# Kernel tuning notes

Hardware: AMD Instinct MI355X
Metric: run time of the kernel (lower is better)

Reference implementation:

```python
import jax, jax.numpy as jnp
import numpy as np

B, C, H, W = 4, 256, 256, 256
P = 256            # num_points
THRESH = 0.8
EPS = 1e-5


def setup_inputs() -> dict:
    key = jax.random.key(0)
    ks = jax.random.split(key, 4)
    x = jax.random.normal(ks[0], (B, C, H, W), dtype=jnp.float32)
    edge = jax.random.uniform(ks[1], (B, 1, H, W), dtype=jnp.float32)
    # GCN params (Conv1d kernel_size=1, no bias) + eval-mode BatchNorm params
    w_adj = jax.random.normal(ks[2], (P, P), dtype=jnp.float32) * (1.0 / np.sqrt(P))
    w_wg = jax.random.normal(ks[3], (C, C), dtype=jnp.float32) * (1.0 / np.sqrt(C))
    return {
        "x": x, "edge": edge,
        "w_adj": w_adj,
        "g_adj": jnp.ones((P,), jnp.float32), "b_adj": jnp.zeros((P,), jnp.float32),
        "m_adj": jnp.zeros((P,), jnp.float32), "v_adj": jnp.ones((P,), jnp.float32),
        "w_wg": w_wg,
        "g_wg": jnp.ones((C,), jnp.float32), "b_wg": jnp.zeros((C,), jnp.float32),
        "m_wg": jnp.zeros((C,), jnp.float32), "v_wg": jnp.ones((C,), jnp.float32),
    }


def _bn(z, mean, var, gamma, beta):
    # eval-mode BatchNorm1d over axis 1 of (B, ch, L)
    inv = gamma / jnp.sqrt(var + EPS)
    return z * inv[None, :, None] + (beta - mean * inv)[None, :, None]


def reference(x, edge, w_adj, g_adj, b_adj, m_adj, v_adj,
              w_wg, g_wg, b_wg, m_wg, v_wg):
    Bx, Cx, Hx, Wx = x.shape
    HW = Hx * Wx
    # threshold boundary map, pick P most-uncertain grid points per image
    e = jnp.where(edge < THRESH, 0.0, edge).reshape(Bx, HW)
    _, idx = jax.lax.top_k(e, P)                      # (B, P) int32 indices into HW
    xf = x.reshape(Bx, Cx, HW)
    idx3 = jnp.broadcast_to(idx[:, None, :], (Bx, Cx, P))
    feat = jnp.take_along_axis(xf, idx3, axis=2)      # gather: (B, C, P)
    feat = feat.transpose(0, 2, 1)                    # (B, P, C) = (b, n, d)
    # GCN stage 1: adjacency mix over nodes + BN + ReLU + residual
    z = jnp.einsum('ij,bjd->bid', w_adj, feat)        # (B, P, C)
    z = jax.nn.relu(_bn(z, m_adj, v_adj, g_adj, b_adj)) + feat
    # GCN stage 2: feature transform + BN + ReLU
    zt = z.transpose(0, 2, 1)                         # (B, C, P)
    z2 = jnp.einsum('cd,bdp->bcp', w_wg, zt)          # (B, C, P)
    z2 = jax.nn.relu(_bn(z2, m_wg, v_wg, g_wg, b_wg))
    # scatter reasoned point features back into the grid (indices are unique per row)
    bi = jnp.arange(Bx)[:, None, None]
    ci = jnp.arange(Cx)[None, :, None]
    out = xf.at[bi, ci, idx3].set(z2)
    return out.reshape(Bx, Cx, Hx, Wx)
```

## Files before the change

### kernel.cpp

```cpp
#include <hip/hip_runtime.h>
#include <stdint.h>

#define HW_   65536
#define B_    4
#define C_    256
#define P_    256
#define TH_   0.8f
#define EPS_  1e-5f

#define CHUNK_  4096
#define NCHUNK_ (HW_ / CHUNK_)
#define NCAND_  (NCHUNK_ * P_)

__device__ __forceinline__ uint64_t make_key(float v, int i) {
    if (v < TH_) v = 0.0f;
    return ((uint64_t)__float_as_uint(v) << 32) | (uint32_t)(65535 - i);
}

__global__ __launch_bounds__(512) void topk_local_kernel(const float* __restrict__ edge,
                                                         uint64_t* __restrict__ cand) {
    __shared__ uint64_t sk[CHUNK_];
    const int b = blockIdx.y;
    const int chunk = blockIdx.x;
    const int tid = threadIdx.x;
    const int base = chunk * CHUNK_;
    for (int t = tid; t < CHUNK_; t += 512) {
        const int i = base + t;
        sk[t] = make_key(edge[b * HW_ + i], i);
    }
    __syncthreads();
    for (int k = 2; k <= CHUNK_; k <<= 1) {
        for (int j = k >> 1; j > 0; j >>= 1) {
            for (int t = tid; t < CHUNK_ / 2; t += 512) {
                const int i = 2 * t - (t & (j - 1));
                const int ixj = i + j;
                const uint64_t a = sk[i], c = sk[ixj];
                const bool desc = ((i & k) == 0);
                if (desc ? (a < c) : (a > c)) { sk[i] = c; sk[ixj] = a; }
            }
            __syncthreads();
        }
    }
    if (tid < 256) cand[(b * NCHUNK_ + chunk) * P_ + tid] = sk[tid];
}

__global__ __launch_bounds__(1024) void topk_merge_kernel(const uint64_t* __restrict__ cand,
                                                          int* __restrict__ idx_out) {
    __shared__ uint64_t sk[NCAND_];
    const int b = blockIdx.x;
    const int tid = threadIdx.x;
    for (int t = tid; t < NCAND_; t += 1024) sk[t] = cand[b * NCAND_ + t];
    __syncthreads();
    for (int k = 2; k <= NCAND_; k <<= 1) {
        for (int j = k >> 1; j > 0; j >>= 1) {
            for (int t = tid; t < NCAND_ / 2; t += 1024) {
                const int i = 2 * t - (t & (j - 1));
                const int ixj = i + j;
                const uint64_t a = sk[i], c = sk[ixj];
                const bool desc = ((i & k) == 0);
                if (desc ? (a < c) : (a > c)) { sk[i] = c; sk[ixj] = a; }
            }
            __syncthreads();
        }
    }
    if (tid < 256) idx_out[b * P_ + tid] = 65535 - (int)(sk[tid] & 0xFFFFFFFFull);
}

__global__ __launch_bounds__(256) void copy_kernel(const float4* __restrict__ src,
                                                   float4* __restrict__ dst, int n4) {
    int i = blockIdx.x * 256 + threadIdx.x;
    const int stride = gridDim.x * 256;
    for (; i < n4; i += stride) dst[i] = src[i];
}

__global__ __launch_bounds__(256) void gather_kernel(const float* __restrict__ x,
                                                     const int* __restrict__ idx,
                                                     float* __restrict__ feat) {
    const int bn = blockIdx.x;
    const int d = threadIdx.x;
    const int b = bn >> 8;
    const int hw = idx[bn];
    feat[(size_t)bn * C_ + d] = x[((size_t)(b * C_ + d)) * HW_ + hw];
}

__global__ __launch_bounds__(256) void mm1_kernel(const float* __restrict__ w_adj,
                                                  const float* __restrict__ feat,
                                                  const float* __restrict__ g,
                                                  const float* __restrict__ bb,
                                                  const float* __restrict__ m,
                                                  const float* __restrict__ vv,
                                                  float* __restrict__ z) {
    __shared__ __align__(16) float a_s[64][68];
    __shared__ __align__(16) float b_s[64][68];
    const int b = blockIdx.y;
    const int i0 = (blockIdx.x >> 2) * 64;
    const int d0 = (blockIdx.x & 3) * 64;
    const int tid = threadIdx.x;
    const int tx = tid & 15, ty = tid >> 4;
    const float* fb = feat + (size_t)b * P_ * C_;

    float acc[4][4] = {};
    for (int k0 = 0; k0 < 256; k0 += 64) {
        for (int l = tid; l < 4096; l += 256) {
            int r = l >> 6, c = l & 63;
            a_s[r][c] = w_adj[(i0 + r) * 256 + (k0 + c)];
            b_s[r][c] = fb[(size_t)(k0 + r) * 256 + (d0 + c)];
        }
        __syncthreads();
        #pragma unroll
        for (int kk = 0; kk < 64; kk += 4) {
            float4 a4[4], b4[4];
            #pragma unroll
            for (int r = 0; r < 4; ++r) a4[r] = *(const float4*)&a_s[ty * 4 + r][kk];
            #pragma unroll
            for (int j = 0; j < 4; ++j) b4[j] = *(const float4*)&b_s[kk + j][tx * 4];
            #pragma unroll
            for (int r = 0; r < 4; ++r) {
                const float4 av = a4[r];
                const float aj0 = av.x, aj1 = av.y, aj2 = av.z, aj3 = av.w;
                acc[r][0] = fmaf(aj0, b4[0].x, acc[r][0]);
                acc[r][1] = fmaf(aj0, b4[0].y, acc[r][1]);
                acc[r][2] = fmaf(aj0, b4[0].z, acc[r][2]);
                acc[r][3] = fmaf(aj0, b4[0].w, acc[r][3]);
                acc[r][0] = fmaf(aj1, b4[1].x, acc[r][0]);
                acc[r][1] = fmaf(aj1, b4[1].y, acc[r][1]);
                acc[r][2] = fmaf(aj1, b4[1].z, acc[r][2]);
                acc[r][3] = fmaf(aj1, b4[1].w, acc[r][3]);
                acc[r][0] = fmaf(aj2, b4[2].x, acc[r][0]);
                acc[r][1] = fmaf(aj2, b4[2].y, acc[r][1]);
                acc[r][2] = fmaf(aj2, b4[2].z, acc[r][2]);
                acc[r][3] = fmaf(aj2, b4[2].w, acc[r][3]);
                acc[r][0] = fmaf(aj3, b4[3].x, acc[r][0]);
                acc[r][1] = fmaf(aj3, b4[3].y, acc[r][1]);
                acc[r][2] = fmaf(aj3, b4[3].z, acc[r][2]);
                acc[r][3] = fmaf(aj3, b4[3].w, acc[r][3]);
            }
        }
        __syncthreads();
    }
    #pragma unroll
    for (int r = 0; r < 4; ++r) {
        const int i = i0 + ty * 4 + r;
        const float inv = g[i] / sqrtf(vv[i] + EPS_);
        const float beta = bb[i] - m[i] * inv;
        const int d = d0 + tx * 4;
        float4 res = *(const float4*)&fb[(size_t)i * 256 + d];
        float4 o;
        o.x = fmaxf(acc[r][0] * inv + beta, 0.0f) + res.x;
        o.y = fmaxf(acc[r][1] * inv + beta, 0.0f) + res.y;
        o.z = fmaxf(acc[r][2] * inv + beta, 0.0f) + res.z;
        o.w = fmaxf(acc[r][3] * inv + beta, 0.0f) + res.w;
        *(float4*)&z[((size_t)b * P_ + i) * C_ + d] = o;
    }
}

__global__ __launch_bounds__(256) void mm2_kernel(const float* __restrict__ w_wg,
                                                  const float* __restrict__ z,
                                                  const int* __restrict__ idx,
                                                  const float* __restrict__ g,
                                                  const float* __restrict__ bb,
                                                  const float* __restrict__ m,
                                                  const float* __restrict__ vv,
                                                  float* __restrict__ out) {
    __shared__ __align__(16) float a_s[64][68];
    __shared__ __align__(16) float bt_s[64][68];
    const int b = blockIdx.y;
    const int c0 = (blockIdx.x >> 2) * 64;
    const int p0 = (blockIdx.x & 3) * 64;
    const int tid = threadIdx.x;
    const int tx = tid & 15, ty = tid >> 4;
    const float* zb = z + (size_t)b * P_ * C_;

    float acc[4][4] = {};
    for (int k0 = 0; k0 < 256; k0 += 64) {
        for (int l = tid; l < 4096; l += 256) {
            int r = l >> 6, c = l & 63;
            a_s[r][c] = w_wg[(c0 + r) * 256 + (k0 + c)];
            bt_s[c][r] = zb[(size_t)(p0 + r) * 256 + (k0 + c)];
        }
        __syncthreads();
        #pragma unroll
        for (int kk = 0; kk < 64; kk += 4) {
            float4 a4[4], b4[4];
            #pragma unroll
            for (int r = 0; r < 4; ++r) a4[r] = *(const float4*)&a_s[ty * 4 + r][kk];
            #pragma unroll
            for (int j = 0; j < 4; ++j) b4[j] = *(const float4*)&bt_s[kk + j][tx * 4];
            #pragma unroll
            for (int r = 0; r < 4; ++r) {
                const float4 av = a4[r];
                const float aj0 = av.x, aj1 = av.y, aj2 = av.z, aj3 = av.w;
                acc[r][0] = fmaf(aj0, b4[0].x, acc[r][0]);
                acc[r][1] = fmaf(aj0, b4[0].y, acc[r][1]);
                acc[r][2] = fmaf(aj0, b4[0].z, acc[r][2]);
                acc[r][3] = fmaf(aj0, b4[0].w, acc[r][3]);
                acc[r][0] = fmaf(aj1, b4[1].x, acc[r][0]);
                acc[r][1] = fmaf(aj1, b4[1].y, acc[r][1]);
                acc[r][2] = fmaf(aj1, b4[1].z, acc[r][2]);
                acc[r][3] = fmaf(aj1, b4[1].w, acc[r][3]);
                acc[r][0] = fmaf(aj2, b4[2].x, acc[r][0]);
                acc[r][1] = fmaf(aj2, b4[2].y, acc[r][1]);
                acc[r][2] = fmaf(aj2, b4[2].z, acc[r][2]);
                acc[r][3] = fmaf(aj2, b4[2].w, acc[r][3]);
                acc[r][0] = fmaf(aj3, b4[3].x, acc[r][0]);
                acc[r][1] = fmaf(aj3, b4[3].y, acc[r][1]);
                acc[r][2] = fmaf(aj3, b4[3].z, acc[r][2]);
                acc[r][3] = fmaf(aj3, b4[3].w, acc[r][3]);
            }
        }
        __syncthreads();
    }
    int pidx[4];
    #pragma unroll
    for (int cc = 0; cc < 4; ++cc) pidx[cc] = idx[b * P_ + p0 + tx * 4 + cc];
    #pragma unroll
    for (int r = 0; r < 4; ++r) {
        const int c = c0 + ty * 4 + r;
        const float inv = g[c] / sqrtf(vv[c] + EPS_);
        const float beta = bb[c] - m[c] * inv;
        float* orow = out + ((size_t)(b * C_ + c)) * HW_;
        #pragma unroll
        for (int cc = 0; cc < 4; ++cc) {
            orow[pidx[cc]] = fmaxf(acc[r][cc] * inv + beta, 0.0f);
        }
    }
}

extern "C" void kernel_launch(void* const* d_in, const int* in_sizes, int n_in,
                              void* d_out, int out_size, void* d_ws, size_t ws_size,
                              hipStream_t stream) {
    const float* x     = (const float*)d_in[0];
    const float* edge  = (const float*)d_in[1];
    const float* w_adj = (const float*)d_in[2];
    const float* g_a   = (const float*)d_in[3];
    const float* b_a   = (const float*)d_in[4];
    const float* m_a   = (const float*)d_in[5];
    const float* v_a   = (const float*)d_in[6];
    const float* w_wg  = (const float*)d_in[7];
    const float* g_w   = (const float*)d_in[8];
    const float* b_w   = (const float*)d_in[9];
    const float* m_w   = (const float*)d_in[10];
    const float* v_w   = (const float*)d_in[11];
    float* out = (float*)d_out;

    char* ws = (char*)d_ws;
    int*      idx  = (int*)ws;
    uint64_t* cand = (uint64_t*)(ws + 4096);
    float*    feat = (float*)(ws + 4096 + (size_t)B_ * NCAND_ * 8);
    float*    z    = feat + (size_t)B_ * P_ * C_;

    copy_kernel<<<4096, 256, 0, stream>>>((const float4*)x, (float4*)out,
                                          (int)((size_t)B_ * C_ * HW_ / 4));

    topk_local_kernel<<<dim3(NCHUNK_, B_), 512, 0, stream>>>(edge, cand);
    topk_merge_kernel<<<B_, 1024, 0, stream>>>(cand, idx);

    gather_kernel<<<B_ * P_, 256, 0, stream>>>(x, idx, feat);

    mm1_kernel<<<dim3(16, B_), 256, 0, stream>>>(w_adj, feat, g_a, b_a, m_a, v_a, z);

    mm2_kernel<<<dim3(16, B_), 256, 0, stream>>>(w_wg, z, idx, g_w, b_w, m_w, v_w, out);
}
```

Before: 612.8 us.

## Replace shared-memory bitonic top-k with register/shuffle sort and max-merge tree

Replaces the full LDS bitonic sort of each 4096-element chunk and of the 4096 candidates with a register-resident bitonic sort of 256-element runs (16 keys per lane, wave shuffles). It then prunes with max-merges that keep only the top 256 at each level. This removes the many __syncthreads-separated LDS passes and the unnecessary full sorts. It adds 64-bit shuffle cost and high register pressure, and correctness depends on the delicate lane-mask merge logic.

```diff
diff --git a/kernel.cpp b/kernel.cpp
--- a/kernel.cpp
+++ b/kernel.cpp
@@ -17,53 +17,167 @@
     return ((uint64_t)__float_as_uint(v) << 32) | (uint32_t)(65535 - i);
 }
 
-__global__ __launch_bounds__(512) void topk_local_kernel(const float* __restrict__ edge,
+__device__ __forceinline__ uint64_t shfl_xor_u64(uint64_t v, int mask) {
+    int lo = __shfl_xor((int)(uint32_t)v, mask, 64);
+    int hi = __shfl_xor((int)(uint32_t)(v >> 32), mask, 64);
+    return ((uint64_t)(uint32_t)hi << 32) | (uint32_t)lo;
+}
+
+__device__ __forceinline__ void ce(uint64_t &a, uint64_t &b, bool desc) {
+    uint64_t x = a, y = b;
+    bool sw = desc ? (x < y) : (x > y);
+    a = sw ? y : x;
+    b = sw ? x : y;
+}
+
+__device__ __forceinline__ void lane_ce16(uint64_t kk[16], int mask, bool want_max) {
+    #pragma unroll
+    for (int e = 0; e < 16; ++e) {
+        uint64_t o = shfl_xor_u64(kk[e], mask);
+        kk[e] = (want_max == (kk[e] > o)) ? kk[e] : o;
+    }
+}
+
+template<int K, int J>
+__device__ __forceinline__ void intra_ce_k(uint64_t kk[16]) {
+    #pragma unroll
+    for (int e = 0; e < 16; ++e)
+        if (!(e & J)) ce(kk[e], kk[e | J], ((e & K) == 0));
+}
+
+template<int J>
+__device__ __forceinline__ void intra_ce(uint64_t kk[16], bool d) {
+    #pragma unroll
+    for (int e = 0; e < 16; ++e)
+        if (!(e & J)) ce(kk[e], kk[e | J], d);
+}
+
+__device__ __forceinline__ void sort256_desc(uint64_t kk[16], int t) {
+    intra_ce_k<2, 1>(kk);
+    intra_ce_k<4, 2>(kk); intra_ce_k<4, 1>(kk);
+    intra_ce_k<8, 4>(kk); intra_ce_k<8, 2>(kk); intra_ce_k<8, 1>(kk);
+    {
+        const bool d = ((t & 1) == 0);
+        intra_ce<8>(kk, d); intra_ce<4>(kk, d); intra_ce<2>(kk, d); intra_ce<1>(kk, d);
+    }
+    {
+        const bool d = ((t & 2) == 0);
+        lane_ce16(kk, 1, ((t & 1) == 0) == d);
+        intra_ce<8>(kk, d); intra_ce<4>(kk, d); intra_ce<2>(kk, d); intra_ce<1>(kk, d);
+    }
+    {
+        const bool d = ((t & 4) == 0);
+        lane_ce16(kk, 2, ((t & 2) == 0) == d);
+        lane_ce16(kk, 1, ((t & 1) == 0) == d);
+        intra_ce<8>(kk, d); intra_ce<4>(kk, d); intra_ce<2>(kk, d); intra_ce<1>(kk, d);
+    }
+    {
+        const bool d = ((t & 8) == 0);
+        lane_ce16(kk, 4, ((t & 4) == 0) == d);
+        lane_ce16(kk, 2, ((t & 2) == 0) == d);
+        lane_ce16(kk, 1, ((t & 1) == 0) == d);
+        intra_ce<8>(kk, d); intra_ce<4>(kk, d); intra_ce<2>(kk, d); intra_ce<1>(kk, d);
+    }
+    lane_ce16(kk, 8, ((t & 8) == 0));
+    lane_ce16(kk, 4, ((t & 4) == 0));
+    lane_ce16(kk, 2, ((t & 2) == 0));
+    lane_ce16(kk, 1, ((t & 1) == 0));
+    intra_ce<8>(kk, true); intra_ce<4>(kk, true); intra_ce<2>(kk, true); intra_ce<1>(kk, true);
+}
+
+__device__ __forceinline__ void merge_desc(uint64_t kk[16], int t) {
+    lane_ce16(kk, 8, ((t & 8) == 0));
+    lane_ce16(kk, 4, ((t & 4) == 0));
+    lane_ce16(kk, 2, ((t & 2) == 0));
+    lane_ce16(kk, 1, ((t & 1) == 0));
+    intra_ce<8>(kk, true); intra_ce<4>(kk, true); intra_ce<2>(kk, true); intra_ce<1>(kk, true);
+}
+
+__device__ __forceinline__ void maxmerge(uint64_t kk[16], int maskL) {
+    uint64_t oth[16];
+    #pragma unroll
+    for (int e = 0; e < 16; ++e)
+        oth[e] = shfl_xor_u64(kk[15 - e], maskL);
+    #pragma unroll
+    for (int e = 0; e < 16; ++e)
+        kk[e] = kk[e] > oth[e] ? kk[e] : oth[e];
+}
+
+__global__ __launch_bounds__(256) void topk_local_kernel(const float* __restrict__ edge,
                                                          uint64_t* __restrict__ cand) {
-    __shared__ uint64_t sk[CHUNK_];
+    __shared__ uint64_t lds[1024];
     const int b = blockIdx.y;
     const int chunk = blockIdx.x;
-    const int tid = threadIdx.x;
+    const int t = threadIdx.x;
     const int base = chunk * CHUNK_;
-    for (int t = tid; t < CHUNK_; t += 512) {
-        const int i = base + t;
-        sk[t] = make_key(edge[b * HW_ + i], i);
+
+    uint64_t kk[16];
+    const float4* ep = (const float4*)(edge + (size_t)b * HW_ + base + t * 16);
+    #pragma unroll
+    for (int q = 0; q < 4; ++q) {
+        const float4 f = ep[q];
+        const int i0 = base + t * 16 + q * 4;
+        kk[q * 4 + 0] = make_key(f.x, i0 + 0);
+        kk[q * 4 + 1] = make_key(f.y, i0 + 1);
+        kk[q * 4 + 2] = make_key(f.z, i0 + 2);
+        kk[q * 4 + 3] = make_key(f.w, i0 + 3);
+    }
+
+    sort256_desc(kk, t);
+    maxmerge(kk, 31); merge_desc(kk, t);
+    maxmerge(kk, 47); merge_desc(kk, t);
+
+    const int w = t >> 6, la = t & 63;
+    if (la < 16) {
+        #pragma unroll
+        for (int e = 0; e < 16; ++e) lds[w * 256 + la * 16 + e] = kk[e];
     }
     __syncthreads();
-    for (int k = 2; k <= CHUNK_; k <<= 1) {
-        for (int j = k >> 1; j > 0; j >>= 1) {
-            for (int t = tid; t < CHUNK_ / 2; t += 512) {
-                const int i = 2 * t - (t & (j - 1));
-                const int ixj = i + j;
-                const uint64_t a = sk[i], c = sk[ixj];
-                const bool desc = ((i & k) == 0);
-                if (desc ? (a < c) : (a > c)) { sk[i] = c; sk[ixj] = a; }
-            }
-            __syncthreads();
-        }
-    }
-    if (tid < 256) cand[(b * NCHUNK_ + chunk) * P_ + tid] = sk[tid];
-}
-
-__global__ __launch_bounds__(1024) void topk_merge_kernel(const uint64_t* __restrict__ cand,
-                                                          int* __restrict__ idx_out) {
-    __shared__ uint64_t sk[NCAND_];
+
+    if (t < 64) {
+        #pragma unroll
+        for (int e = 0; e < 16; ++e) kk[e] = lds[t * 16 + e];
+        maxmerge(kk, 31); merge_desc(kk, t);
+        maxmerge(kk, 47); merge_desc(kk, t);
+        if (t < 16) {
+            #pragma unroll
+            for (int e = 0; e < 16; ++e)
+                cand[((size_t)(b * NCHUNK_ + chunk)) * P_ + t * 16 + e] = kk[e];
+        }
+    }
+}
+
+__global__ __launch_bounds__(256) void topk_merge_kernel(const uint64_t* __restrict__ cand,
+                                                         int* __restrict__ idx_out) {
+    __shared__ uint64_t lds[1024];
     const int b = blockIdx.x;
-    const int tid = threadIdx.x;
-    for (int t = tid; t < NCAND_; t += 1024) sk[t] = cand[b * NCAND_ + t];
+    const int t = threadIdx.x;
+
+    uint64_t kk[16];
+    #pragma unroll
+    for (int e = 0; e < 16; ++e) kk[e] = cand[(size_t)b * NCAND_ + t * 16 + e];
+
+    maxmerge(kk, 31); merge_desc(kk, t);
+    maxmerge(kk, 47); merge_desc(kk, t);
+
+    const int w = t >> 6, la = t & 63;
+    if (la < 16) {
+        #pragma unroll
+        for (int e = 0; e < 16; ++e) lds[w * 256 + la * 16 + e] = kk[e];
+    }
     __syncthreads();
-    for (int k = 2; k <= NCAND_; k <<= 1) {
-        for (int j = k >> 1; j > 0; j >>= 1) {
-            for (int t = tid; t < NCAND_ / 2; t += 1024) {
-                const int i = 2 * t - (t & (j - 1));
-                const int ixj = i + j;
-                const uint64_t a = sk[i], c = sk[ixj];
-                const bool desc = ((i & k) == 0);
-                if (desc ? (a < c) : (a > c)) { sk[i] = c; sk[ixj] = a; }
-            }
-            __syncthreads();
-        }
-    }
-    if (tid < 256) idx_out[b * P_ + tid] = 65535 - (int)(sk[tid] & 0xFFFFFFFFull);
+
+    if (t < 64) {
+        #pragma unroll
+        for (int e = 0; e < 16; ++e) kk[e] = lds[t * 16 + e];
+        maxmerge(kk, 31); merge_desc(kk, t);
+        maxmerge(kk, 47); merge_desc(kk, t);
+        if (t < 16) {
+            #pragma unroll
+            for (int e = 0; e < 16; ++e)
+                idx_out[b * P_ + t * 16 + e] = 65535 - (int)(kk[e] & 0xFFFFFFFFull);
+        }
+    }
 }
 
 __global__ __launch_bounds__(256) void copy_kernel(const float4* __restrict__ src,
@@ -252,8 +366,8 @@
     copy_kernel<<<4096, 256, 0, stream>>>((const float4*)x, (float4*)out,
                                           (int)((size_t)B_ * C_ * HW_ / 4));
 
-    topk_local_kernel<<<dim3(NCHUNK_, B_), 512, 0, stream>>>(edge, cand);
-    topk_merge_kernel<<<B_, 1024, 0, stream>>>(cand, idx);
+    topk_local_kernel<<<dim3(NCHUNK_, B_), 256, 0, stream>>>(edge, cand);
+    topk_merge_kernel<<<B_, 256, 0, stream>>>(cand, idx);
 
     gather_kernel<<<B_ * P_, 256, 0, stream>>>(x, idx, feat);
 
```

New measurement: 688.3 us. 1.12x slower.
